# Kernel optimization log

Measured on AMD Instinct MI355X. Metric: run time of the kernel, lower is better.

Reference implementation:

```python
import math
import jax, jax.numpy as jnp
import numpy as np

B, T, HID = 8, 2048, 1536
H, D = 8, 192
CHUNK, PAST, FUT = 12, 12, 0
CTX = CHUNK + PAST + FUT          # 24
F = PAST + FUT + 1                # 13 relative positions
CAP = 50.0
INVALID = -1.0e9


def setup_inputs() -> dict:
    key = jax.random.key(0)
    k1, k2, k3 = jax.random.split(key, 3)
    x = jax.random.normal(k1, (B, T, HID), dtype=jnp.float32)
    mask = jnp.zeros((B, T), dtype=bool)  # True = invalid/padding
    # causal validity: key offset (c - PAST) relative to query w must lie in [-PAST, FUT]
    w = jnp.arange(CHUNK)[:, None]
    c = jnp.arange(CTX)[None, :]
    causal_valid_mask = (c >= w) & (c <= w + PAST + FUT)  # [CHUNK, CTX]
    W_qkv = jax.random.normal(k2, (HID, 3 * HID), dtype=jnp.float32) * 0.02
    W_pos = jax.random.normal(k3, (HID, HID), dtype=jnp.float32) * 0.02
    per_dim_scale = jnp.zeros((D,), dtype=jnp.float32)
    return {"x": x, "mask": mask, "causal_valid_mask": causal_valid_mask,
            "W_qkv": W_qkv, "W_pos": W_pos, "per_dim_scale": per_dim_scale}


def _extract_block_context(z, U):
    # pad time dim left=PAST, right=FUT+CHUNK-1, then frame with step CHUNK, len CTX
    pad = ((0, 0), (PAST, FUT + CHUNK - 1)) + ((0, 0),) * (z.ndim - 2)
    zp = jnp.pad(z, pad)
    idx = jnp.arange(U)[:, None] * CHUNK + jnp.arange(CTX)[None, :]  # [U, CTX]
    return zp[:, idx]  # [B, U, CTX, ...]


def reference(x, mask, causal_valid_mask, W_qkv, W_pos, per_dim_scale):
    b, t, _ = x.shape
    qkv = x @ W_qkv
    q, k, v = jnp.split(qkv, 3, axis=-1)
    q = q.reshape(b, t, H, D)
    k = k.reshape(b, t, H, D)
    v = v.reshape(b, t, H, D)

    q_scale = D ** (-0.5) / math.log(2.0)
    k_scale = math.log(1.0 + math.e) / math.log(2.0)
    q = q * q_scale * jax.nn.softplus(per_dim_scale)  # per-dim scale on queries
    k = k * k_scale

    U = -(-t // CHUNK)  # ceil
    pad_q = U * CHUNK - t
    qb = jnp.pad(q, ((0, 0), (0, pad_q), (0, 0), (0, 0))).reshape(b, U, CHUNK, H, D)
    kb = _extract_block_context(k, U)            # [B,U,CTX,H,D]
    vb = _extract_block_context(v, U)            # [B,U,CTX,H,D]
    valid = _extract_block_context(~mask, U)     # [B,U,CTX]

    # ---- relative position embedding (Transformer-XL style) ----
    pos = jnp.arange(PAST, -FUT - 1, -1, dtype=jnp.float32)  # [F]
    nts = HID // 2
    inv_ts = jnp.exp(jnp.arange(nts, dtype=jnp.float32) * (-(math.log(10000.0) / (nts - 1))))
    st = pos[:, None] * inv_ts[None, :]
    emb = jnp.concatenate([jnp.sin(st), jnp.cos(st)], axis=-1)  # [F, HID]
    sin_emb = (emb @ W_pos).reshape(F, H, D)

    term_ac = jnp.einsum('buwhd,buchd->bhuwc', qb, kb)     # content-content
    term_bd = jnp.einsum('buwhd,fhd->bhuwf', qb, sin_emb)  # content-position
    # relative shift: pad last dim to CTX+1, flatten, slice, reshape
    pad_amt = CTX + 1 - F
    tb = jnp.pad(term_bd, ((0, 0),) * 4 + ((0, pad_amt),))
    tb = tb.reshape(b, H, U, CHUNK * (CTX + 1))[..., :CHUNK * CTX]
    tb = tb.reshape(b, H, U, CHUNK, CTX)

    logits = term_ac + tb
    logits = jnp.tanh(logits / CAP) * CAP  # softcap
    cond = valid[:, None, :, None, :] & causal_valid_mask[None, None, None, :, :]
    logits = jnp.where(cond, logits, INVALID)
    probs = jax.nn.softmax(logits, axis=-1)
    out = jnp.einsum('bhuwc,buchd->buwhd', probs, vb)
    return out.reshape(b, U * CHUNK, H, D)[:, :t]
```

## Files before the change

kernel.cpp:

```cpp
#include <hip/hip_runtime.h>

typedef unsigned int u32;
typedef unsigned short u16;

typedef __attribute__((ext_vector_type(8))) short bf16x8;
typedef __attribute__((ext_vector_type(4))) float f32x4;

__device__ __forceinline__ u16 f2bf(float f) {
  u32 u = __builtin_bit_cast(u32, f);
  u32 r = (u + 0x7fffu + ((u >> 16) & 1u)) >> 16;
  return (u16)r;
}
__device__ __forceinline__ float bfl(u32 u) { return __builtin_bit_cast(float, u << 16); }
__device__ __forceinline__ float bfh(u32 u) { return __builtin_bit_cast(float, u & 0xffff0000u); }

__device__ __forceinline__ void gload_lds16(const u16* g, u16* l) {
  __builtin_amdgcn_global_load_lds(
      (const __attribute__((address_space(1))) void*)g,
      (__attribute__((address_space(3))) void*)l, 16, 0, 0);
}

__global__ __launch_bounds__(256) void transp_wt(const float* __restrict__ W,
                                                 u16* __restrict__ Wt) {
  __shared__ float tile[64][68];
  int bk = blockIdx.x % 24, bn = blockIdx.x / 24;
  int k0 = bk * 64, n0 = bn * 64;
  int tid = threadIdx.x;
#pragma unroll
  for (int p = 0; p < 4; p++) {
    int idx = p * 256 + tid;
    int r = idx >> 4, c4 = idx & 15;
    *(float4*)&tile[r][c4 * 4] = *(const float4*)&W[(size_t)(k0 + r) * 4608 + n0 + c4 * 4];
  }
  __syncthreads();
#pragma unroll
  for (int p = 0; p < 2; p++) {
    int idx = p * 256 + tid;
    int rn = idx >> 3, kc = idx & 7;
    u16 pk[8];
#pragma unroll
    for (int e = 0; e < 8; e++) pk[e] = f2bf(tile[kc * 8 + e][rn]);
    *(uint4*)&Wt[(size_t)(n0 + rn) * 1536 + k0 + kc * 8] = *(const uint4*)pk;
  }
}

__global__ __launch_bounds__(256) void conv_x(const float* __restrict__ X,
                                              u16* __restrict__ Xb) {
  int i = blockIdx.x * 256 + threadIdx.x;
  const float4* xp = (const float4*)X;
  float4 a = xp[i * 2], b = xp[i * 2 + 1];
  uint4 o;
  o.x = (u32)f2bf(a.x) | ((u32)f2bf(a.y) << 16);
  o.y = (u32)f2bf(a.z) | ((u32)f2bf(a.w) << 16);
  o.z = (u32)f2bf(b.x) | ((u32)f2bf(b.y) << 16);
  o.w = (u32)f2bf(b.z) | ((u32)f2bf(b.w) << 16);
  ((uint4*)Xb)[i] = o;
}

__global__ __launch_bounds__(256) void pos_emb_part(const float* __restrict__ Wp,
                                                    float* __restrict__ part) {
  __shared__ float er[13 * 32];
  int ks = blockIdx.x % 48, nb = blockIdx.x / 48;
  int tid = threadIdx.x;
  int n = nb * 256 + tid;
  const float cfreq = 9.210340371976184f / 767.0f;
  for (int i = tid; i < 13 * 32; i += 256) {
    int f = i >> 5, kk = i & 31;
    int k = ks * 32 + kk;
    int ii = (k < 768) ? k : (k - 768);
    float fr = expf(-cfreq * (float)ii);
    float st = (float)(12 - f) * fr;
    er[f * 32 + kk] = (k < 768) ? sinf(st) : cosf(st);
  }
  __syncthreads();
  float acc[13];
#pragma unroll
  for (int f = 0; f < 13; f++) acc[f] = 0.f;
  const float* wp = Wp + (size_t)(ks * 32) * 1536 + n;
  for (int kk = 0; kk < 32; kk++) {
    float w = wp[(size_t)kk * 1536];
#pragma unroll
    for (int f = 0; f < 13; f++) acc[f] = fmaf(er[f * 32 + kk], w, acc[f]);
  }
#pragma unroll
  for (int f = 0; f < 13; f++)
    part[((size_t)ks * 13 + f) * 1536 + n] = acc[f];
}

__global__ __launch_bounds__(256) void pos_emb_red(const float* __restrict__ part,
                                                   u16* __restrict__ sembbf) {
  int idxg = blockIdx.x * 256 + threadIdx.x;
  int f = idxg / 1536, n = idxg % 1536;
  float s = 0.f;
  if (f < 13)
    for (int ks = 0; ks < 48; ks++)
      s += part[((size_t)ks * 13 + f) * 1536 + n];
  sembbf[idxg] = f2bf(s);
}

__global__ __launch_bounds__(512, 2) void gemm_qkv(const u16* __restrict__ Xb,
                                                   const u16* __restrict__ Bt,
                                                   u16* __restrict__ C,
                                                   const float* __restrict__ pds) {
  extern __shared__ u16 smem[];

  const int tid = threadIdx.x;
  const int lane = tid & 63;
  const int wv = tid >> 6;
  const int wr = wv >> 1;
  const int wc = wv & 1;
  const int lr = lane & 15;
  const int lkq = lane >> 4;
  const int sx = lr & 7;

  int bid = blockIdx.x;
  int xcd = bid & 7, idx = bid >> 3;
  int bm = xcd * 8 + idx / 16;
  int bn = idx % 16;
  int m0 = bm * 256, n0 = bn * 288;

  auto stageA = [&](int T) {
#pragma unroll
    for (int q = 0; q < 4; q++) {
      int ch = q * 512 + tid;
      int r = ch >> 3, cr = ch & 7;
      int crs = cr ^ (r & 7);
      const u16* g = Xb + (size_t)(m0 + r) * 1536 + T * 64 + crs * 8;
      u16* l = smem + (T & 1) * 34816 + ch * 8;
      gload_lds16(g, l);
    }
  };
  auto stageB = [&](int T) {
#pragma unroll
    for (int q = 0; q < 4; q++) {
      int ch = q * 512 + tid;
      int r = ch >> 3, cr = ch & 7;
      int crs = cr ^ (r & 7);
      const u16* g = Bt + (size_t)(n0 + r) * 1536 + T * 64 + crs * 8;
      u16* l = smem + (T & 1) * 34816 + 16384 + ch * 8;
      gload_lds16(g, l);
    }
    if (tid < 256) {
      int ch = 2048 + tid;
      int r = ch >> 3, cr = ch & 7;
      int crs = cr ^ (r & 7);
      const u16* g = Bt + (size_t)(n0 + r) * 1536 + T * 64 + crs * 8;
      u16* l = smem + (T & 1) * 34816 + 16384 + ch * 8;
      gload_lds16(g, l);
    }
  };

  f32x4 acc[4][9];
#pragma unroll
  for (int i = 0; i < 4; i++)
#pragma unroll
    for (int j = 0; j < 9; j++) acc[i][j] = (f32x4){0.f, 0.f, 0.f, 0.f};

  stageA(0); stageB(0);
  asm volatile("s_waitcnt vmcnt(0)" ::: "memory");
  __builtin_amdgcn_s_barrier();

  bf16x8 af[8], bfr[6];

  for (int t = 0; t < 24; t++) {
    const int b = (t & 1) * 34816;

#pragma unroll
    for (int i = 0; i < 4; i++)
#pragma unroll
      for (int ks = 0; ks < 2; ks++) {
        int R = wr * 64 + i * 16 + lr;
        af[i * 2 + ks] = *(const bf16x8*)&smem[b + R * 64 + ((ks * 4 + lkq) ^ sx) * 8];
      }
#pragma unroll
    for (int j = 0; j < 3; j++)
#pragma unroll
      for (int ks = 0; ks < 2; ks++) {
        int R = wc * 144 + j * 16 + lr;
        bfr[j * 2 + ks] = *(const bf16x8*)&smem[b + 16384 + R * 64 + ((ks * 4 + lkq) ^ sx) * 8];
      }
    if (t < 23) { stageA(t + 1); stageB(t + 1); }
    __builtin_amdgcn_s_barrier();
    __builtin_amdgcn_s_setprio(1);
#pragma unroll
    for (int i = 0; i < 4; i++)
#pragma unroll
      for (int j = 0; j < 3; j++)
#pragma unroll
        for (int ks = 0; ks < 2; ks++)
          acc[i][j] = __builtin_amdgcn_mfma_f32_16x16x32_bf16(af[i * 2 + ks], bfr[j * 2 + ks], acc[i][j], 0, 0, 0);
    __builtin_amdgcn_s_setprio(0);
    __builtin_amdgcn_s_barrier();

#pragma unroll
    for (int j = 0; j < 3; j++)
#pragma unroll
      for (int ks = 0; ks < 2; ks++) {
        int R = wc * 144 + (3 + j) * 16 + lr;
        bfr[j * 2 + ks] = *(const bf16x8*)&smem[b + 16384 + R * 64 + ((ks * 4 + lkq) ^ sx) * 8];
      }
    __builtin_amdgcn_s_barrier();
    __builtin_amdgcn_s_setprio(1);
#pragma unroll
    for (int i = 0; i < 4; i++)
#pragma unroll
      for (int j = 0; j < 3; j++)
#pragma unroll
        for (int ks = 0; ks < 2; ks++)
          acc[i][3 + j] = __builtin_amdgcn_mfma_f32_16x16x32_bf16(af[i * 2 + ks], bfr[j * 2 + ks], acc[i][3 + j], 0, 0, 0);
    __builtin_amdgcn_s_setprio(0);
    __builtin_amdgcn_s_barrier();

#pragma unroll
    for (int j = 0; j < 3; j++)
#pragma unroll
      for (int ks = 0; ks < 2; ks++) {
        int R = wc * 144 + (6 + j) * 16 + lr;
        bfr[j * 2 + ks] = *(const bf16x8*)&smem[b + 16384 + R * 64 + ((ks * 4 + lkq) ^ sx) * 8];
      }
    __builtin_amdgcn_s_barrier();
    __builtin_amdgcn_s_setprio(1);
#pragma unroll
    for (int i = 0; i < 4; i++)
#pragma unroll
      for (int j = 0; j < 3; j++)
#pragma unroll
        for (int ks = 0; ks < 2; ks++)
          acc[i][6 + j] = __builtin_amdgcn_mfma_f32_16x16x32_bf16(af[i * 2 + ks], bfr[j * 2 + ks], acc[i][6 + j], 0, 0, 0);
    __builtin_amdgcn_s_setprio(0);
    asm volatile("s_waitcnt vmcnt(0)" ::: "memory");
    __builtin_amdgcn_s_barrier();
  }

  const float kscale = 1.8946361f;
  float scl[9];
#pragma unroll
  for (int j = 0; j < 9; j++) {
    int gcol = n0 + wc * 144 + j * 16 + lr;
    float s;
    if (gcol < 1536) s = 0.10411754f * log1pf(expf(pds[gcol % 192]));
    else if (gcol < 3072) s = kscale;
    else s = 1.0f;
    scl[j] = s;
  }
  int r0 = lkq * 4;
#pragma unroll
  for (int i = 0; i < 4; i++)
#pragma unroll
    for (int j = 0; j < 9; j++) {
      int row = wr * 64 + i * 16 + r0;
      int col = wc * 144 + j * 16 + lr;
#pragma unroll
      for (int r = 0; r < 4; r++)
        smem[(row + r) * 296 + col] = f2bf(acc[i][j][r] * scl[j]);
    }
  asm volatile("s_waitcnt lgkmcnt(0)" ::: "memory");
  __builtin_amdgcn_s_barrier();
#pragma unroll
  for (int p = 0; p < 18; p++) {
    int idx2 = p * 512 + tid;
    int row = idx2 / 36, cq = idx2 % 36;
    *(uint4*)&C[(size_t)(m0 + row) * 4608 + n0 + cq * 8] =
        *(const uint4*)&smem[row * 296 + cq * 8];
  }
}

__global__ __launch_bounds__(512) void qsemb(const u16* __restrict__ qkv,
                                             const u16* __restrict__ sembbf,
                                             float* __restrict__ bdall) {
  int tid = threadIdx.x;
  int lane = tid & 63;
  int h = tid >> 6;
  int t0 = blockIdx.x * 16;
  int arow = lane & 15, ak = lane >> 4;

  const u16* qp = qkv + (size_t)(t0 + arow) * 4608 + h * 192 + ak * 8;
  const u16* sp = sembbf + (size_t)(lane & 15) * 1536 + h * 192 + ak * 8;

  f32x4 acc = (f32x4){0.f, 0.f, 0.f, 0.f};
#pragma unroll
  for (int kt = 0; kt < 6; kt++) {
    bf16x8 a = *(const bf16x8*)(qp + kt * 32);
    bf16x8 bb = *(const bf16x8*)(sp + kt * 32);
    acc = __builtin_amdgcn_mfma_f32_16x16x32_bf16(a, bb, acc, 0, 0, 0);
  }
  int f = lane & 15;
  int rbase = (lane >> 4) * 4;
  if (f < 13) {
#pragma unroll
    for (int r = 0; r < 4; r++)
      bdall[(size_t)(t0 + rbase + r) * 104 + h * 13 + f] = acc[r];
  }
}

__global__ __launch_bounds__(256) void attn_kernel(const u16* __restrict__ qkv,
                                                   const float* __restrict__ bdall,
                                                   const unsigned char* __restrict__ mask,
                                                   float* __restrict__ out) {
  __shared__ u16 sq[24 * 200];
  __shared__ u16 sk[36 * 200];
  __shared__ u16 sv[36 * 200];
  __shared__ float lg[24 * 14];
  __shared__ int vld[36];

  int bid = blockIdx.x;
  int h = bid & 7;
  int u2 = (bid >> 3) % 86;
  int b = bid / (86 * 8);
  int tid = threadIdx.x;
  int tbase = u2 * 24;

  if (tid < 36) {
    int t = tbase + tid - 12;
    vld[tid] = (t >= 0 && t < 2048 && mask[b * 2048 + t] == 0) ? 1 : 0;
  }

  const u16* base = qkv + (size_t)b * 2048 * 4608 + h * 192;
  for (int idx = tid; idx < 576; idx += 256) {
    int w = idx / 24, g = idx % 24;
    int t = tbase + w;
    uint4 val = {0u, 0u, 0u, 0u};
    if (t < 2048) val = *(const uint4*)(base + (size_t)t * 4608 + g * 8);
    *(uint4*)&sq[w * 200 + g * 8] = val;
  }
  for (int idx = tid; idx < 1728; idx += 256) {
    int kv = idx / 864, r = idx % 864;
    int c = r / 24, g = r % 24;
    int t = tbase + c - 12;
    uint4 val = {0u, 0u, 0u, 0u};
    if (t >= 0 && t < 2048)
      val = *(const uint4*)(base + (size_t)t * 4608 + (kv ? 3072 : 1536) + g * 8);
    if (kv) *(uint4*)&sv[c * 200 + g * 8] = val;
    else    *(uint4*)&sk[c * 200 + g * 8] = val;
  }
  __syncthreads();

  for (int idx = tid; idx < 312; idx += 256) {
    int w = idx % 24, f = idx / 24;
    int c = w + f;
    int t = tbase + w;
    float l = -1e9f;
    if (vld[c] && t < 2048) {
      float ac = 0.f;
      const u16* qp = &sq[w * 200];
      const u16* kp = &sk[c * 200];
#pragma unroll 4
      for (int i = 0; i < 24; i++) {
        uint4 qa = *(const uint4*)(qp + i * 8);
        uint4 kb = *(const uint4*)(kp + i * 8);
        ac = fmaf(bfl(qa.x), bfl(kb.x), ac);
        ac = fmaf(bfh(qa.x), bfh(kb.x), ac);
        ac = fmaf(bfl(qa.y), bfl(kb.y), ac);
        ac = fmaf(bfh(qa.y), bfh(kb.y), ac);
        ac = fmaf(bfl(qa.z), bfl(kb.z), ac);
        ac = fmaf(bfh(qa.z), bfh(kb.z), ac);
        ac = fmaf(bfl(qa.w), bfl(kb.w), ac);
        ac = fmaf(bfh(qa.w), bfh(kb.w), ac);
      }
      float bd = bdall[(size_t)(b * 2048 + t) * 104 + h * 13 + f];
      l = tanhf((ac + bd) * 0.02f) * 50.f;
    }
    lg[w * 14 + f] = l;
  }
  __syncthreads();

  if (tid < 24) {
    float m = -3e38f;
#pragma unroll
    for (int f = 0; f < 13; f++) m = fmaxf(m, lg[tid * 14 + f]);
    float s = 0.f;
#pragma unroll
    for (int f = 0; f < 13; f++) {
      float e = expf(lg[tid * 14 + f] - m);
      lg[tid * 14 + f] = e;
      s += e;
    }
    float inv = 1.f / s;
#pragma unroll
    for (int f = 0; f < 13; f++) lg[tid * 14 + f] *= inv;
  }
  __syncthreads();

  for (int idx = tid; idx < 1152; idx += 256) {
    int w = idx / 48, g = idx % 48;
    int t = tbase + w;
    if (t >= 2048) continue;
    float a0 = 0, a1 = 0, a2 = 0, a3 = 0;
#pragma unroll
    for (int f = 0; f < 13; f++) {
      float p = lg[w * 14 + f];
      uint2 vv = *(const uint2*)&sv[(w + f) * 200 + g * 4];
      a0 = fmaf(p, bfl(vv.x), a0);
      a1 = fmaf(p, bfh(vv.x), a1);
      a2 = fmaf(p, bfl(vv.y), a2);
      a3 = fmaf(p, bfh(vv.y), a3);
    }
    float4 o = {a0, a1, a2, a3};
    *(float4*)&out[(((size_t)(b * 2048 + t)) * 8 + h) * 192 + g * 4] = o;
  }
}

extern "C" void kernel_launch(void* const* d_in, const int* in_sizes, int n_in,
                              void* d_out, int out_size, void* d_ws, size_t ws_size,
                              hipStream_t stream) {
  (void)in_sizes; (void)n_in; (void)out_size; (void)ws_size;
  const float* x = (const float*)d_in[0];
  const unsigned char* mask = (const unsigned char*)d_in[1];
  const float* Wqkv = (const float*)d_in[3];
  const float* Wpos = (const float*)d_in[4];
  const float* pds = (const float*)d_in[5];
  float* out = (float*)d_out;

  char* ws = (char*)d_ws;
  u16* Wt = (u16*)ws;
  u16* qkv = (u16*)(ws + 14155776);
  u16* Xb = (u16*)(ws + 165150720);
  u16* sembbf = (u16*)(ws + 215482368);
  float* bdall = (float*)(ws + 215531520);
  float* part = (float*)(ws + 222347264);

  transp_wt<<<1728, 256, 0, stream>>>(Wqkv, Wt);
  conv_x<<<12288, 256, 0, stream>>>(x, Xb);
  pos_emb_part<<<288, 256, 0, stream>>>(Wpos, part);
  pos_emb_red<<<96, 256, 0, stream>>>(part, sembbf);
  gemm_qkv<<<1024, 512, 151552, stream>>>(Xb, Wt, qkv, pds);
  qsemb<<<1024, 512, 0, stream>>>(qkv, sembbf, bdall);
  attn_kernel<<<5504, 256, 0, stream>>>(qkv, bdall, mask, out);
}
```

Measured before the change: 370.2 us.

## Retile QKV GEMM to 256x192 with triple-buffered A and deeper prefetch

The QKV GEMM tile changes from 256x288 to 256x192, and the wave layout goes from 4x2 to 2x4 waves. Each wave now computes a 128x48 sub-tile in two phases per k-step instead of three. The A tile is triple-buffered and B double-buffered, with loads issued two k-steps ahead and partial vmcnt waits, so memory latency overlaps more with MFMA work. The grid grows to 1536 blocks with slightly less LDS per block, but the wave tile is less square, which raises LDS fragment traffic per MFMA.

```diff
diff --git a/kernel.cpp b/kernel.cpp
--- a/kernel.cpp
+++ b/kernel.cpp
@@ -107,17 +107,17 @@
   const int tid = threadIdx.x;
   const int lane = tid & 63;
   const int wv = tid >> 6;
-  const int wr = wv >> 1;
-  const int wc = wv & 1;
+  const int wr = wv >> 2;
+  const int wc = wv & 3;
   const int lr = lane & 15;
   const int lkq = lane >> 4;
   const int sx = lr & 7;
 
   int bid = blockIdx.x;
   int xcd = bid & 7, idx = bid >> 3;
-  int bm = xcd * 8 + idx / 16;
-  int bn = idx % 16;
-  int m0 = bm * 256, n0 = bn * 288;
+  int bm = xcd * 8 + idx / 24;
+  int bn = idx % 24;
+  int m0 = bm * 256, n0 = bn * 192;
 
   auto stageA = [&](int T) {
 #pragma unroll
@@ -126,60 +126,53 @@
       int r = ch >> 3, cr = ch & 7;
       int crs = cr ^ (r & 7);
       const u16* g = Xb + (size_t)(m0 + r) * 1536 + T * 64 + crs * 8;
-      u16* l = smem + (T & 1) * 34816 + ch * 8;
+      u16* l = smem + (T % 3) * 16384 + ch * 8;
       gload_lds16(g, l);
     }
   };
   auto stageB = [&](int T) {
 #pragma unroll
-    for (int q = 0; q < 4; q++) {
+    for (int q = 0; q < 3; q++) {
       int ch = q * 512 + tid;
       int r = ch >> 3, cr = ch & 7;
       int crs = cr ^ (r & 7);
       const u16* g = Bt + (size_t)(n0 + r) * 1536 + T * 64 + crs * 8;
-      u16* l = smem + (T & 1) * 34816 + 16384 + ch * 8;
+      u16* l = smem + 49152 + (T & 1) * 12288 + ch * 8;
       gload_lds16(g, l);
     }
-    if (tid < 256) {
-      int ch = 2048 + tid;
-      int r = ch >> 3, cr = ch & 7;
-      int crs = cr ^ (r & 7);
-      const u16* g = Bt + (size_t)(n0 + r) * 1536 + T * 64 + crs * 8;
-      u16* l = smem + (T & 1) * 34816 + 16384 + ch * 8;
-      gload_lds16(g, l);
-    }
   };
 
-  f32x4 acc[4][9];
-#pragma unroll
-  for (int i = 0; i < 4; i++)
-#pragma unroll
-    for (int j = 0; j < 9; j++) acc[i][j] = (f32x4){0.f, 0.f, 0.f, 0.f};
-
-  stageA(0); stageB(0);
-  asm volatile("s_waitcnt vmcnt(0)" ::: "memory");
+  f32x4 acc[8][3];
+#pragma unroll
+  for (int i = 0; i < 8; i++)
+#pragma unroll
+    for (int j = 0; j < 3; j++) acc[i][j] = (f32x4){0.f, 0.f, 0.f, 0.f};
+
+  stageA(0); stageB(0); stageA(1); stageB(1);
+  asm volatile("s_waitcnt vmcnt(7)" ::: "memory");
   __builtin_amdgcn_s_barrier();
 
   bf16x8 af[8], bfr[6];
 
   for (int t = 0; t < 24; t++) {
-    const int b = (t & 1) * 34816;
-
+    const int ab = (t % 3) * 16384;
+    const int bb = 49152 + (t & 1) * 12288;
+
+#pragma unroll
+    for (int j = 0; j < 3; j++)
+#pragma unroll
+      for (int ks = 0; ks < 2; ks++) {
+        int R = wc * 48 + j * 16 + lr;
+        bfr[j * 2 + ks] = *(const bf16x8*)&smem[bb + R * 64 + ((ks * 4 + lkq) ^ sx) * 8];
+      }
 #pragma unroll
     for (int i = 0; i < 4; i++)
 #pragma unroll
       for (int ks = 0; ks < 2; ks++) {
-        int R = wr * 64 + i * 16 + lr;
-        af[i * 2 + ks] = *(const bf16x8*)&smem[b + R * 64 + ((ks * 4 + lkq) ^ sx) * 8];
+        int R = wr * 128 + i * 16 + lr;
+        af[i * 2 + ks] = *(const bf16x8*)&smem[ab + R * 64 + ((ks * 4 + lkq) ^ sx) * 8];
       }
-#pragma unroll
-    for (int j = 0; j < 3; j++)
-#pragma unroll
-      for (int ks = 0; ks < 2; ks++) {
-        int R = wc * 144 + j * 16 + lr;
-        bfr[j * 2 + ks] = *(const bf16x8*)&smem[b + 16384 + R * 64 + ((ks * 4 + lkq) ^ sx) * 8];
-      }
-    if (t < 23) { stageA(t + 1); stageB(t + 1); }
+    if (t < 22) stageA(t + 2);
     __builtin_amdgcn_s_barrier();
     __builtin_amdgcn_s_setprio(1);
 #pragma unroll
@@ -193,12 +186,13 @@
     __builtin_amdgcn_s_barrier();
 
 #pragma unroll
-    for (int j = 0; j < 3; j++)
+    for (int i = 0; i < 4; i++)
 #pragma unroll
       for (int ks = 0; ks < 2; ks++) {
-        int R = wc * 144 + (3 + j) * 16 + lr;
-        bfr[j * 2 + ks] = *(const bf16x8*)&smem[b + 16384 + R * 64 + ((ks * 4 + lkq) ^ sx) * 8];
+        int R = wr * 128 + 64 + i * 16 + lr;
+        af[i * 2 + ks] = *(const bf16x8*)&smem[ab + R * 64 + ((ks * 4 + lkq) ^ sx) * 8];
       }
+    if (t < 22) stageB(t + 2);
     __builtin_amdgcn_s_barrier();
     __builtin_amdgcn_s_setprio(1);
 #pragma unroll
@@ -207,36 +201,21 @@
       for (int j = 0; j < 3; j++)
 #pragma unroll
         for (int ks = 0; ks < 2; ks++)
-          acc[i][3 + j] = __builtin_amdgcn_mfma_f32_16x16x32_bf16(af[i * 2 + ks], bfr[j * 2 + ks], acc[i][3 + j], 0, 0, 0);
+          acc[4 + i][j] = __builtin_amdgcn_mfma_f32_16x16x32_bf16(af[i * 2 + ks], bfr[j * 2 + ks], acc[4 + i][j], 0, 0, 0);
     __builtin_amdgcn_s_setprio(0);
+    if (t < 22) {
+      asm volatile("s_waitcnt vmcnt(7)" ::: "memory");
+    } else {
+      asm volatile("s_waitcnt vmcnt(0)" ::: "memory");
+    }
     __builtin_amdgcn_s_barrier();
-
-#pragma unroll
-    for (int j = 0; j < 3; j++)
-#pragma unroll
-      for (int ks = 0; ks < 2; ks++) {
-        int R = wc * 144 + (6 + j) * 16 + lr;
-        bfr[j * 2 + ks] = *(const bf16x8*)&smem[b + 16384 + R * 64 + ((ks * 4 + lkq) ^ sx) * 8];
-      }
-    __builtin_amdgcn_s_barrier();
-    __builtin_amdgcn_s_setprio(1);
-#pragma unroll
-    for (int i = 0; i < 4; i++)
-#pragma unroll
-      for (int j = 0; j < 3; j++)
-#pragma unroll
-        for (int ks = 0; ks < 2; ks++)
-          acc[i][6 + j] = __builtin_amdgcn_mfma_f32_16x16x32_bf16(af[i * 2 + ks], bfr[j * 2 + ks], acc[i][6 + j], 0, 0, 0);
-    __builtin_amdgcn_s_setprio(0);
-    asm volatile("s_waitcnt vmcnt(0)" ::: "memory");
-    __builtin_amdgcn_s_barrier();
   }
 
   const float kscale = 1.8946361f;
-  float scl[9];
-#pragma unroll
-  for (int j = 0; j < 9; j++) {
-    int gcol = n0 + wc * 144 + j * 16 + lr;
+  float scl[3];
+#pragma unroll
+  for (int j = 0; j < 3; j++) {
+    int gcol = n0 + wc * 48 + j * 16 + lr;
     float s;
     if (gcol < 1536) s = 0.10411754f * log1pf(expf(pds[gcol % 192]));
     else if (gcol < 3072) s = kscale;
@@ -245,23 +224,23 @@
   }
   int r0 = lkq * 4;
 #pragma unroll
-  for (int i = 0; i < 4; i++)
-#pragma unroll
-    for (int j = 0; j < 9; j++) {
-      int row = wr * 64 + i * 16 + r0;
-      int col = wc * 144 + j * 16 + lr;
+  for (int i = 0; i < 8; i++)
+#pragma unroll
+    for (int j = 0; j < 3; j++) {
+      int row = wr * 128 + i * 16 + r0;
+      int col = wc * 48 + j * 16 + lr;
 #pragma unroll
       for (int r = 0; r < 4; r++)
-        smem[(row + r) * 296 + col] = f2bf(acc[i][j][r] * scl[j]);
+        smem[(row + r) * 200 + col] = f2bf(acc[i][j][r] * scl[j]);
     }
   asm volatile("s_waitcnt lgkmcnt(0)" ::: "memory");
   __builtin_amdgcn_s_barrier();
 #pragma unroll
-  for (int p = 0; p < 18; p++) {
+  for (int p = 0; p < 12; p++) {
     int idx2 = p * 512 + tid;
-    int row = idx2 / 36, cq = idx2 % 36;
+    int row = idx2 / 24, cq = idx2 % 24;
     *(uint4*)&C[(size_t)(m0 + row) * 4608 + n0 + cq * 8] =
-        *(const uint4*)&smem[row * 296 + cq * 8];
+        *(const uint4*)&smem[row * 200 + cq * 8];
   }
 }
 
@@ -423,7 +402,7 @@
   conv_x<<<12288, 256, 0, stream>>>(x, Xb);
   pos_emb_part<<<288, 256, 0, stream>>>(Wpos, part);
   pos_emb_red<<<96, 256, 0, stream>>>(part, sembbf);
-  gemm_qkv<<<1024, 512, 151552, stream>>>(Xb, Wt, qkv, pds);
+  gemm_qkv<<<1536, 512, 147456, stream>>>(Xb, Wt, qkv, pds);
   qsemb<<<1024, 512, 0, stream>>>(qkv, sembbf, bdall);
   attn_kernel<<<5504, 256, 0, stream>>>(qkv, bdall, mask, out);
 }
```

Result: faster. 358.6 us (-3.1%).
